# Performance work log

Hardware: AMD Instinct MI355X
Metric: run time of the kernel (lower is better)

## Reference

```python
import jax, jax.numpy as jnp
import numpy as np

ROPE_THETA = 500000.0


def apply_rope(x, position_ids):
    # x: (B, H, S, hd), position_ids: (B, S)
    hd = x.shape[-1]
    inv_freq = 1.0 / (ROPE_THETA ** (jnp.arange(0, hd, 2, dtype=x.dtype) / hd))  # (hd/2,)
    freqs = position_ids.astype(x.dtype)[:, :, None] * inv_freq  # (B, S, hd/2)
    sin = jnp.sin(freqs)[:, None, :, :]  # (B, 1, S, hd/2)
    cos = jnp.cos(freqs)[:, None, :, :]
    x1 = x[..., ::2]
    x2 = x[..., 1::2]
    even = x1 * cos - x2 * sin
    odd = x2 * cos + x1 * sin
    # interleave even/odd back: stack on a new trailing axis then flatten
    return jnp.stack([even, odd], axis=-1).reshape(x.shape)


def setup_inputs() -> dict:
    key = jax.random.key(0)
    k_x, k_q, k_k, k_v, k_o = jax.random.split(key, 5)
    B, S, D = 2, 2048, 2048
    H, H_kv = 32, 8
    hd = D // H
    x = jax.random.normal(k_x, (B, S, D), dtype=jnp.float32)
    position_ids = jnp.broadcast_to(jnp.arange(S, dtype=jnp.int64)[None, :], (B, S))
    scale = 0.02
    Wq = jax.random.normal(k_q, (D, H * hd), dtype=jnp.float32) * scale
    Wk = jax.random.normal(k_k, (D, H_kv * hd), dtype=jnp.float32) * scale
    Wv = jax.random.normal(k_v, (D, H_kv * hd), dtype=jnp.float32) * scale
    Wo = jax.random.normal(k_o, (D, D), dtype=jnp.float32) * scale
    return {"x": x, "position_ids": position_ids, "Wq": Wq, "Wk": Wk, "Wv": Wv, "Wo": Wo}


def reference(x, position_ids, Wq, Wk, Wv, Wo):
    B, S, D = x.shape
    H, H_kv = 32, 8
    hd = D // H
    G = H // H_kv  # query heads per kv head

    q = (x @ Wq).reshape(B, S, H, hd).transpose(0, 2, 1, 3)        # (B, H, S, hd)
    k = (x @ Wk).reshape(B, S, H_kv, hd).transpose(0, 2, 1, 3)     # (B, H_kv, S, hd)
    v = (x @ Wv).reshape(B, S, H_kv, hd).transpose(0, 2, 1, 3)

    q = apply_rope(q, position_ids)
    k = apply_rope(k, position_ids)

    # GQA: group query heads (B, H_kv, G, S, hd); repeat_interleave maps head h -> kv head h // G
    qg = q.reshape(B, H_kv, G, S, hd)
    scores = jnp.einsum("bkgsh,bkth->bkgst", qg, k) / jnp.sqrt(jnp.asarray(hd, x.dtype))

    causal = jnp.triu(jnp.ones((S, S), dtype=bool), 1)  # True = masked
    scores = jnp.where(causal, jnp.asarray(-jnp.inf, scores.dtype), scores)

    attn = jax.nn.softmax(scores, axis=-1)  # (B, H_kv, G, S, S)
    z = jnp.einsum("bkgst,bkth->bkgsh", attn, v)  # (B, H_kv, G, S, hd)
    z = z.reshape(B, H, S, hd).transpose(0, 2, 1, 3).reshape(B, S, D)
    return z @ Wo
```

## Files before the change

### kernel.cpp

```cpp
#include <hip/hip_runtime.h>
#include <hip/hip_bf16.h>


#define S_LEN 2048
#define DIM   2048
#define NH    32
#define NKV   8
#define HD    64
#define BS    4096
#define NQKV  3072
#define LL(x) ((long long)(x))

typedef __bf16 bf16x8 __attribute__((ext_vector_type(8)));
typedef float  f32x4  __attribute__((ext_vector_type(4)));
typedef float  f32x16 __attribute__((ext_vector_type(16)));
typedef unsigned u32x4 __attribute__((ext_vector_type(4)));

__device__ __forceinline__ unsigned short bfb(float f) {
  __hip_bfloat16 h = __float2bfloat16(f);
  return *reinterpret_cast<unsigned short*>(&h);
}

__device__ __forceinline__ unsigned cvtpk(float lo, float hi) {
  unsigned u;
  asm("v_cvt_pk_bf16_f32 %0, %1, %2" : "=v"(u) : "v"(lo), "v"(hi));
  return u;
}

__device__ __forceinline__ float fmax3(float a, float b, float c) {
  float d;
  asm("v_max3_f32 %0, %1, %2, %3" : "=v"(d) : "v"(a), "v"(b), "v"(c));
  return d;
}

__device__ __forceinline__ void gload16(const void* g, void* l) {
  __builtin_amdgcn_global_load_lds(
      (const __attribute__((address_space(1))) void*)g,
      (__attribute__((address_space(3))) void*)l, 16, 0, 0);
}

__device__ __forceinline__ void tcast_body(
    const float* __restrict__ in, unsigned short* __restrict__ out,
    int K, int N, int bx, int by, int tid, float* tile ) {
  int n0 = bx * 32, k0 = by * 32;
  int tx = tid & 31, ty = tid >> 5;
#pragma unroll
  for (int r = 0; r < 32; r += 8)
    tile[(ty + r) * 33 + tx] = in[LL(k0 + ty + r) * N + n0 + tx];
  __syncthreads();
#pragma unroll
  for (int r = 0; r < 32; r += 8)
    out[LL(n0 + ty + r) * K + k0 + tx] = bfb(tile[tx * 33 + ty + r]);
}

__global__ __launch_bounds__(256) void k_prep(
    const float* __restrict__ x,  const float* __restrict__ Wq,
    const float* __restrict__ Wk, const float* __restrict__ Wv,
    const float* __restrict__ Wo, float* __restrict__ tab,
    unsigned short* __restrict__ xb, unsigned short* __restrict__ wqkvt,
    unsigned short* __restrict__ wot) {
  __shared__ float tile[32 * 33];
  int blk = blockIdx.x, tid = threadIdx.x;
  if (blk < 256) {
    int i = blk * 256 + tid;
    int s = i >> 5, f = i & 31;
    double inv = pow(500000.0, -2.0 * (double)f / 64.0);
    double fr = (double)s * inv;
    tab[2 * i]     = (float)cos(fr);
    tab[2 * i + 1] = (float)sin(fr);
  } else if (blk < 8448) {
    int i = (blk - 256) * 256 + tid;
    float4 v = ((const float4*)x)[i];
    ushort4 o;
    o.x = bfb(v.x); o.y = bfb(v.y); o.z = bfb(v.z); o.w = bfb(v.w);
    ((ushort4*)xb)[i] = o;
  } else if (blk < 12544) {
    int t2 = blk - 8448;
    tcast_body(Wq, wqkvt, DIM, DIM, t2 & 63, t2 >> 6, tid, tile);
  } else if (blk < 13568) {
    int t3 = blk - 12544;
    tcast_body(Wk, wqkvt + LL(2048) * DIM, DIM, 512, t3 & 15, t3 >> 4, tid, tile);
  } else if (blk < 14592) {
    int t4 = blk - 13568;
    tcast_body(Wv, wqkvt + LL(2560) * DIM, DIM, 512, t4 & 15, t4 >> 4, tid, tile);
  } else {
    int t5 = blk - 14592;
    tcast_body(Wo, wot, DIM, DIM, t5 & 63, t5 >> 6, tid, tile);
  }
}

__global__ void k_vtrans(const unsigned short* __restrict__ vbuf, unsigned short* __restrict__ vt) {
  __shared__ __align__(16) unsigned short tile[64][72];
  int s0 = blockIdx.x * 64;
  int bh = blockIdx.y;
  int b = bh >> 3, kvh = bh & 7;
  int t = threadIdx.x;
#pragma unroll
  for (int c = t; c < 512; c += 256) {
    int s = c >> 3, seg = c & 7;
    *(uint4*)&tile[s][seg * 8] =
        *(const uint4*)(vbuf + LL(b * S_LEN + s0 + s) * (NKV * HD) + kvh * HD + seg * 8);
  }
  __syncthreads();
#pragma unroll
  for (int c = t; c < 512; c += 256) {
    int d = c >> 3, sseg = c & 7;
    ushort4 x0, x1;
    unsigned short* xp = (unsigned short*)&x0;
#pragma unroll
    for (int j = 0; j < 4; j++) xp[j] = tile[sseg * 8 + j][d];
    unsigned short* yp = (unsigned short*)&x1;
#pragma unroll
    for (int j = 0; j < 4; j++) yp[j] = tile[sseg * 8 + 4 + j][d];
    uint4 o;
    o.x = ((unsigned*)&x0)[0]; o.y = ((unsigned*)&x0)[1];
    o.z = ((unsigned*)&x1)[0]; o.w = ((unsigned*)&x1)[1];
    *(uint4*)(vt + (LL(bh) * HD + d) * S_LEN + s0 + sseg * 8) = o;
  }
}

template <int MODE>
__global__ __launch_bounds__(256, 2) void k_gemm(
    const unsigned short* __restrict__ A, const unsigned short* __restrict__ Bt,
    void* __restrict__ Cout, int M, int N, int K,
    const float* __restrict__ tab, unsigned short* __restrict__ qbuf,
    unsigned short* __restrict__ kbuf, unsigned short* __restrict__ vbuf) {
  __shared__ __align__(16) unsigned short As[128 * 32];
  __shared__ __align__(16) unsigned short Bs[128 * 32];
  int t = threadIdx.x;
  int lane = t & 63, w = t >> 6;
  int wr = w >> 1, wc = w & 1;
  int g = lane >> 4, r = lane & 15;
  int gx = gridDim.x;
  int nwg = gx * gridDim.y;
  int lin = blockIdx.y * gx + blockIdx.x;
  int cpx = nwg >> 3;
  int swz = (lin & 7) * cpx + (lin >> 3);
  int bx = swz % gx, by = swz / gx;
  long long rowBase = LL(by) * 128;
  long long colBase = LL(bx) * 128;

  f32x4 acc[4][4] = {};

  int c0 = t, c1 = t + 256;
  const unsigned short* ag0 = A + (rowBase + (c0 >> 2)) * K + (c0 & 3) * 8;
  const unsigned short* ag1 = A + (rowBase + (c1 >> 2)) * K + (c1 & 3) * 8;
  const unsigned short* bg0 = Bt + (colBase + (c0 >> 2)) * K + (c0 & 3) * 8;
  const unsigned short* bg1 = Bt + (colBase + (c1 >> 2)) * K + (c1 & 3) * 8;
  char* lA0 = (char*)As + c0 * 16; char* lA1 = (char*)As + c1 * 16;
  char* lB0 = (char*)Bs + c0 * 16; char* lB1 = (char*)Bs + c1 * 16;

  for (int kt = 0; kt < K; kt += 32) {
    __syncthreads();
    gload16(ag0 + kt, lA0);
    gload16(ag1 + kt, lA1);
    gload16(bg0 + kt, lB0);
    gload16(bg1 + kt, lB1);
    __syncthreads();

    bf16x8 af[4], bfr[4];
#pragma unroll
    for (int m = 0; m < 4; m++)
      af[m] = *(const bf16x8*)(const void*)(As + (wr * 64 + m * 16 + r) * 32 + g * 8);
#pragma unroll
    for (int n = 0; n < 4; n++)
      bfr[n] = *(const bf16x8*)(const void*)(Bs + (wc * 64 + n * 16 + r) * 32 + g * 8);
#pragma unroll
    for (int m = 0; m < 4; m++)
#pragma unroll
      for (int n = 0; n < 4; n++)
        acc[m][n] = __builtin_amdgcn_mfma_f32_16x16x32_bf16(af[m], bfr[n], acc[m][n], 0, 0, 0);
  }

  if (MODE == 0) {
#pragma unroll
    for (int m = 0; m < 4; m++)
#pragma unroll
      for (int n = 0; n < 4; n++) {
        long long row0 = rowBase + wr * 64 + m * 16 + g * 4;
        long long col = colBase + wc * 64 + n * 16 + r;
#pragma unroll
        for (int j = 0; j < 4; j++)
          ((float*)Cout)[(row0 + j) * N + col] = acc[m][n][j];
      }
  } else {
#pragma unroll
    for (int n = 0; n < 4; n++) {
      int gc0 = (int)colBase + wc * 64 + n * 16;
      int gc = gc0 + r;
      unsigned short* dst; int dcol, dstride; float scale; bool rope;
      if (gc0 < 2048)      { dst = qbuf; dcol = gc;        dstride = DIM; scale = 0.18033688f; rope = true; }
      else if (gc0 < 2560) { dst = kbuf; dcol = gc - 2048; dstride = 512; scale = 1.0f;        rope = true; }
      else                 { dst = vbuf; dcol = gc - 2560; dstride = 512; scale = 1.0f;        rope = false; }
      int f = (gc & 63) >> 1;
      float sgn = (gc & 1) ? 1.f : -1.f;
#pragma unroll
      for (int m = 0; m < 4; m++) {
        long long row0 = rowBase + wr * 64 + m * 16 + g * 4;
#pragma unroll
        for (int j = 0; j < 4; j++) {
          float v = acc[m][n][j];
          float o;
          if (rope) {
            float part = __shfl_xor(v, 1);
            int s = (int)((row0 + j) & (S_LEN - 1));
            float cc = tab[(s * 32 + f) * 2], ss = tab[(s * 32 + f) * 2 + 1];
            o = (v * cc + sgn * part * ss) * scale;
          } else o = v;
          dst[(row0 + j) * dstride + dcol] = bfb(o);
        }
      }
    }
  }
}

__global__ __launch_bounds__(256, 2) void k_attn(
    const unsigned short* __restrict__ qb, const unsigned short* __restrict__ kb,
    const unsigned short* __restrict__ vt, unsigned short* __restrict__ zb) {
  int lin = blockIdx.x + 8 * (blockIdx.y + 32 * blockIdx.z);
  int kvh = lin & 7;
  int idx = lin >> 3;
  int b = idx >> 5;
  int j = idx & 31;
  int h = kvh * 4 + (j & 3);
  int pair = j >> 2;
  int bh = b * NKV + kvh;

  int t = threadIdx.x, lane = t & 63, w = t >> 6;
  int l31 = lane & 31, hi = lane >> 5;
  int sw = (l31 & 7) * 8;

  __shared__ __align__(16) unsigned short Ks[2][64 * 64];
  __shared__ __align__(16) unsigned short Vs[2][64 * 64];

  int c0 = t, c1 = t + 256;
  const unsigned short* kg0 = kb + LL(b) * S_LEN * 512 + (c0 >> 3) * 512 + kvh * HD
                                 + (((c0 & 7) ^ ((c0 >> 3) & 7)) * 8);
  const unsigned short* kg1 = kb + LL(b) * S_LEN * 512 + (c1 >> 3) * 512 + kvh * HD
                                 + (((c1 & 7) ^ ((c1 >> 3) & 7)) * 8);
  const unsigned short* vg0 = vt + (LL(bh) * HD + (c0 >> 3)) * S_LEN
                                 + (((c0 & 7) ^ ((c0 >> 3) & 7)) * 8);
  const unsigned short* vg1 = vt + (LL(bh) * HD + (c1 >> 3)) * S_LEN
                                 + (((c1 & 7) ^ ((c1 >> 3) & 7)) * 8);

#define STAGE(bufi, kst_)                                              \
  {                                                                    \
    gload16(kg0 + LL(kst_) * 512, (char*)Ks[bufi] + c0 * 16);          \
    gload16(kg1 + LL(kst_) * 512, (char*)Ks[bufi] + c1 * 16);          \
    gload16(vg0 + (kst_), (char*)Vs[bufi] + c0 * 16);                  \
    gload16(vg1 + (kst_), (char*)Vs[bufi] + c1 * 16);                  \
  }

#pragma unroll 1
  for (int pass = 0; pass < 2; pass++) {
    int st = pass ? (15 - pair) : pair;
    int rowb = st * 128 + w * 32;
    int qg = rowb + l31;
    long long qrow = LL(b) * S_LEN + qg;

    bf16x8 qf[4];
#pragma unroll
    for (int s = 0; s < 4; s++)
      qf[s] = *(const bf16x8*)(const void*)(qb + qrow * DIM + h * HD + s * 16 + hi * 8);

    f32x16 acc0 = {}, acc1 = {};
    float mrun = -1e30f, lrun = 0.f;

    int nt = 2 * st + 2;
    __syncthreads();
    STAGE(0, 0);
    for (int tt = 0; tt < nt; tt++) {
      int kst = tt * 64;
      int cur = tt & 1;
      if (tt + 1 < nt) {
        STAGE(cur ^ 1, kst + 64);
        asm volatile("s_waitcnt vmcnt(4)" ::: "memory");
      } else {
        asm volatile("s_waitcnt vmcnt(0)" ::: "memory");
      }
      __builtin_amdgcn_s_barrier();
      __builtin_amdgcn_sched_barrier(0);

      if (kst <= rowb + 31) {
        const unsigned short* Kc = Ks[cur];
        const unsigned short* Vc = Vs[cur];

        bf16x8 kf[2][4];
#pragma unroll
        for (int kbi = 0; kbi < 2; kbi++)
#pragma unroll
          for (int s = 0; s < 4; s++)
            kf[kbi][s] = *(const bf16x8*)(const void*)(
                Kc + (kbi * 32 + l31) * 64 + ((s * 16 + hi * 8) ^ sw));

        __builtin_amdgcn_s_setprio(1);
        f32x16 sc0 = {}, sc1 = {};
#pragma unroll
        for (int s = 0; s < 4; s++) {
          sc0 = __builtin_amdgcn_mfma_f32_32x32x16_bf16(kf[0][s], qf[s], sc0, 0, 0, 0);
          sc1 = __builtin_amdgcn_mfma_f32_32x32x16_bf16(kf[1][s], qf[s], sc1, 0, 0, 0);
        }
        __builtin_amdgcn_s_setprio(0);

        bf16x8 vf[8];
#pragma unroll
        for (int db = 0; db < 2; db++)
#pragma unroll
          for (int f = 0; f < 4; f++)
            vf[db * 4 + f] = *(const bf16x8*)(const void*)(
                Vc + (db * 32 + l31) * 64 + ((f * 16 + hi * 8) ^ sw));

        if (kst + 63 > rowb) {
#pragma unroll
          for (int q = 0; q < 16; q++) {
            int kl = (q & 3) + 8 * (q >> 2) + 4 * hi;
            if (kst + kl > qg) sc0[q] = -1e30f;
            if (kst + 32 + kl > qg) sc1[q] = -1e30f;
          }
        }

        float tq[16];
#pragma unroll
        for (int q = 0; q < 16; q++) tq[q] = fmaxf(sc0[q], sc1[q]);
        float u0 = fmax3(tq[0], tq[1], tq[2]);
        float u1 = fmax3(tq[3], tq[4], tq[5]);
        float u2 = fmax3(tq[6], tq[7], tq[8]);
        float u3 = fmax3(tq[9], tq[10], tq[11]);
        float u4 = fmax3(tq[12], tq[13], tq[14]);
        float lpm = fmaxf(fmax3(u0, u1, u2), fmax3(u3, u4, tq[15]));
        if (__any(lpm > mrun + 12.0f)) {
          float pmr = fmaxf(lpm, __shfl_xor(lpm, 32));
          float mnew = fmaxf(mrun, pmr);
          float al = exp2f(mrun - mnew);
          mrun = mnew;
          lrun *= al;
          acc0 *= al;
          acc1 *= al;
        }
        f32x16 pv0, pv1;
#pragma unroll
        for (int q = 0; q < 16; q++) {
          pv0[q] = exp2f(sc0[q] - mrun);
          pv1[q] = exp2f(sc1[q] - mrun);
        }
        {
          float la = 0.f, lb = 0.f, lc = 0.f, ld = 0.f;
#pragma unroll
          for (int q = 0; q < 16; q += 4) {
            la += pv0[q];     lb += pv0[q + 1];
            lc += pv0[q + 2]; ld += pv0[q + 3];
            la += pv1[q];     lb += pv1[q + 1];
            lc += pv1[q + 2]; ld += pv1[q + 3];
          }
          lrun += (la + lb) + (lc + ld);
        }

        bf16x8 pfr[4];
#pragma unroll
        for (int f = 0; f < 4; f++) {
          int qb_ = (f & 1) * 8;
          float e0, e1, e2, e3, e4, e5, e6, e7;
          if (f < 2) {
            e0 = pv0[qb_ + 0]; e1 = pv0[qb_ + 1]; e2 = pv0[qb_ + 2]; e3 = pv0[qb_ + 3];
            e4 = pv0[qb_ + 4]; e5 = pv0[qb_ + 5]; e6 = pv0[qb_ + 6]; e7 = pv0[qb_ + 7];
          } else {
            e0 = pv1[qb_ + 0]; e1 = pv1[qb_ + 1]; e2 = pv1[qb_ + 2]; e3 = pv1[qb_ + 3];
            e4 = pv1[qb_ + 4]; e5 = pv1[qb_ + 5]; e6 = pv1[qb_ + 6]; e7 = pv1[qb_ + 7];
          }
          unsigned a0 = cvtpk(e0, e1), a1 = cvtpk(e2, e3);
          unsigned b0 = cvtpk(e4, e5), b1 = cvtpk(e6, e7);
          unsigned y0 = __shfl_xor(hi ? a0 : b0, 32);
          unsigned y1 = __shfl_xor(hi ? a1 : b1, 32);
          u32x4 uu;
          uu[0] = hi ? y0 : a0;
          uu[1] = hi ? y1 : a1;
          uu[2] = hi ? b0 : y0;
          uu[3] = hi ? b1 : y1;
          pfr[f] = *(bf16x8*)&uu;
        }

        __builtin_amdgcn_s_setprio(1);
#pragma unroll
        for (int f = 0; f < 4; f++) {
          acc0 = __builtin_amdgcn_mfma_f32_32x32x16_bf16(vf[f],     pfr[f], acc0, 0, 0, 0);
          acc1 = __builtin_amdgcn_mfma_f32_32x32x16_bf16(vf[4 + f], pfr[f], acc1, 0, 0, 0);
        }
        __builtin_amdgcn_s_setprio(0);
      }

      __builtin_amdgcn_sched_barrier(0);
      __builtin_amdgcn_s_barrier();
    }

    float lfull = lrun + __shfl_xor(lrun, 32);
    float invl = 1.0f / lfull;
#pragma unroll
    for (int q4 = 0; q4 < 4; q4++) {
      uint2 u;
      u.x = cvtpk(acc0[q4 * 4 + 0] * invl, acc0[q4 * 4 + 1] * invl);
      u.y = cvtpk(acc0[q4 * 4 + 2] * invl, acc0[q4 * 4 + 3] * invl);
      *(uint2*)(void*)(zb + qrow * DIM + h * HD + 8 * q4 + 4 * hi) = u;
      uint2 v;
      v.x = cvtpk(acc1[q4 * 4 + 0] * invl, acc1[q4 * 4 + 1] * invl);
      v.y = cvtpk(acc1[q4 * 4 + 2] * invl, acc1[q4 * 4 + 3] * invl);
      *(uint2*)(void*)(zb + qrow * DIM + h * HD + 32 + 8 * q4 + 4 * hi) = v;
    }
  }
#undef STAGE
}

extern "C" void kernel_launch(void* const* d_in, const int* in_sizes, int n_in,
                              void* d_out, int out_size, void* d_ws, size_t ws_size,
                              hipStream_t stream) {
  const float* x  = (const float*)d_in[0];
  const float* Wq = (const float*)d_in[2];
  const float* Wk = (const float*)d_in[3];
  const float* Wv = (const float*)d_in[4];
  const float* Wo = (const float*)d_in[5];
  float* out = (float*)d_out;

  char* wsb = (char*)d_ws;
  size_t off = 0;
  auto alloc = [&](size_t bytes) {
    void* p = wsb + off;
    off += (bytes + 255) & ~(size_t)255;
    return p;
  };
  float* tab            = (float*)alloc(LL(S_LEN) * 32 * 2 * 4);
  unsigned short* xb    = (unsigned short*)alloc(LL(BS) * DIM * 2);
  unsigned short* wqkvt = (unsigned short*)alloc(LL(NQKV) * DIM * 2);
  unsigned short* wot   = (unsigned short*)alloc(LL(DIM) * DIM * 2);
  unsigned short* qbuf  = (unsigned short*)alloc(LL(BS) * DIM * 2);
  unsigned short* kbuf  = (unsigned short*)alloc(LL(BS) * (NKV * HD) * 2);
  unsigned short* vbuf  = (unsigned short*)alloc(LL(BS) * (NKV * HD) * 2);
  unsigned short* vtb   = (unsigned short*)alloc(LL(2 * NKV) * HD * S_LEN * 2);
  unsigned short* zb    = (unsigned short*)alloc(LL(BS) * DIM * 2);

  k_prep<<<18688, 256, 0, stream>>>(x, Wq, Wk, Wv, Wo, tab, xb, wqkvt, wot);

  k_gemm<2><<<dim3(NQKV / 128, BS / 128), 256, 0, stream>>>(
      xb, wqkvt, nullptr, BS, NQKV, DIM, tab, qbuf, kbuf, vbuf);

  k_vtrans<<<dim3(S_LEN / 64, 2 * NKV), 256, 0, stream>>>(vbuf, vtb);

  k_attn<<<dim3(8, NH, 2), 256, 0, stream>>>(qbuf, kbuf, vtb, zb);

  k_gemm<0><<<dim3(DIM / 128, BS / 128), 256, 0, stream>>>(
      zb, wot, out, BS, DIM, DIM, nullptr, nullptr, nullptr, nullptr);
}
```

Baseline: 221.8 us.

## Fuse V transpose into QKV GEMM epilogue and simplify softmax max/sum reduction

The QKV projection epilogue now writes V directly in transposed (head, dim, seq) layout, which removes the separate k_vtrans kernel launch and the intermediate vbuf round trip. The transposed stores are strided by S_LEN per element, so the GEMM epilogue gets scattered 2-byte writes in place of row-contiguous ones. The attention softmax also replaces the max3 tree with a linear fmax chain, shuffles the row max before the rescale check, and reduces the row sum across half-waves on every tile instead of once at the end. That moves one shuffle per tile into the inner loop and lengthens the dependency chains.

```diff
diff --git a/kernel.cpp b/kernel.cpp
--- a/kernel.cpp
+++ b/kernel.cpp
@@ -25,12 +25,6 @@
   unsigned u;
   asm("v_cvt_pk_bf16_f32 %0, %1, %2" : "=v"(u) : "v"(lo), "v"(hi));
   return u;
-}
-
-__device__ __forceinline__ float fmax3(float a, float b, float c) {
-  float d;
-  asm("v_max3_f32 %0, %1, %2, %3" : "=v"(d) : "v"(a), "v"(b), "v"(c));
-  return d;
 }
 
 __device__ __forceinline__ void gload16(const void* g, void* l) {
@@ -89,42 +83,12 @@
   }
 }
 
-__global__ void k_vtrans(const unsigned short* __restrict__ vbuf, unsigned short* __restrict__ vt) {
-  __shared__ __align__(16) unsigned short tile[64][72];
-  int s0 = blockIdx.x * 64;
-  int bh = blockIdx.y;
-  int b = bh >> 3, kvh = bh & 7;
-  int t = threadIdx.x;
-#pragma unroll
-  for (int c = t; c < 512; c += 256) {
-    int s = c >> 3, seg = c & 7;
-    *(uint4*)&tile[s][seg * 8] =
-        *(const uint4*)(vbuf + LL(b * S_LEN + s0 + s) * (NKV * HD) + kvh * HD + seg * 8);
-  }
-  __syncthreads();
-#pragma unroll
-  for (int c = t; c < 512; c += 256) {
-    int d = c >> 3, sseg = c & 7;
-    ushort4 x0, x1;
-    unsigned short* xp = (unsigned short*)&x0;
-#pragma unroll
-    for (int j = 0; j < 4; j++) xp[j] = tile[sseg * 8 + j][d];
-    unsigned short* yp = (unsigned short*)&x1;
-#pragma unroll
-    for (int j = 0; j < 4; j++) yp[j] = tile[sseg * 8 + 4 + j][d];
-    uint4 o;
-    o.x = ((unsigned*)&x0)[0]; o.y = ((unsigned*)&x0)[1];
-    o.z = ((unsigned*)&x1)[0]; o.w = ((unsigned*)&x1)[1];
-    *(uint4*)(vt + (LL(bh) * HD + d) * S_LEN + s0 + sseg * 8) = o;
-  }
-}
-
 template <int MODE>
 __global__ __launch_bounds__(256, 2) void k_gemm(
     const unsigned short* __restrict__ A, const unsigned short* __restrict__ Bt,
     void* __restrict__ Cout, int M, int N, int K,
     const float* __restrict__ tab, unsigned short* __restrict__ qbuf,
-    unsigned short* __restrict__ kbuf, unsigned short* __restrict__ vbuf) {
+    unsigned short* __restrict__ kbuf, unsigned short* __restrict__ vtb) {
   __shared__ __align__(16) unsigned short As[128 * 32];
   __shared__ __align__(16) unsigned short Bs[128 * 32];
   int t = threadIdx.x;
@@ -188,26 +152,37 @@
     for (int n = 0; n < 4; n++) {
       int gc0 = (int)colBase + wc * 64 + n * 16;
       int gc = gc0 + r;
-      unsigned short* dst; int dcol, dstride; float scale; bool rope;
-      if (gc0 < 2048)      { dst = qbuf; dcol = gc;        dstride = DIM; scale = 0.18033688f; rope = true; }
-      else if (gc0 < 2560) { dst = kbuf; dcol = gc - 2048; dstride = 512; scale = 1.0f;        rope = true; }
-      else                 { dst = vbuf; dcol = gc - 2560; dstride = 512; scale = 1.0f;        rope = false; }
-      int f = (gc & 63) >> 1;
-      float sgn = (gc & 1) ? 1.f : -1.f;
-#pragma unroll
-      for (int m = 0; m < 4; m++) {
-        long long row0 = rowBase + wr * 64 + m * 16 + g * 4;
-#pragma unroll
-        for (int j = 0; j < 4; j++) {
-          float v = acc[m][n][j];
-          float o;
-          if (rope) {
+      if (gc0 < 2560) {
+        unsigned short* dst; int dcol, dstride; float scale;
+        if (gc0 < 2048) { dst = qbuf; dcol = gc;        dstride = DIM; scale = 0.18033688f; }
+        else            { dst = kbuf; dcol = gc - 2048; dstride = 512; scale = 1.0f; }
+        int f = (gc & 63) >> 1;
+        float sgn = (gc & 1) ? 1.f : -1.f;
+#pragma unroll
+        for (int m = 0; m < 4; m++) {
+          long long row0 = rowBase + wr * 64 + m * 16 + g * 4;
+#pragma unroll
+          for (int j = 0; j < 4; j++) {
+            float v = acc[m][n][j];
             float part = __shfl_xor(v, 1);
             int s = (int)((row0 + j) & (S_LEN - 1));
             float cc = tab[(s * 32 + f) * 2], ss = tab[(s * 32 + f) * 2 + 1];
-            o = (v * cc + sgn * part * ss) * scale;
-          } else o = v;
-          dst[(row0 + j) * dstride + dcol] = bfb(o);
+            float o = (v * cc + sgn * part * ss) * scale;
+            dst[(row0 + j) * dstride + dcol] = bfb(o);
+          }
+        }
+      } else {
+        int dcol = gc - 2560;
+#pragma unroll
+        for (int m = 0; m < 4; m++) {
+          long long row0 = rowBase + wr * 64 + m * 16 + g * 4;
+#pragma unroll
+          for (int j = 0; j < 4; j++) {
+            long long row = row0 + j;
+            long long bq = row >> 11;
+            int s = (int)(row & (S_LEN - 1));
+            vtb[(bq * 512 + dcol) * S_LEN + s] = bfb(acc[m][n][j]);
+          }
         }
       }
     }
@@ -319,18 +294,15 @@
           }
         }
 
-        float tq[16];
-#pragma unroll
-        for (int q = 0; q < 16; q++) tq[q] = fmaxf(sc0[q], sc1[q]);
-        float u0 = fmax3(tq[0], tq[1], tq[2]);
-        float u1 = fmax3(tq[3], tq[4], tq[5]);
-        float u2 = fmax3(tq[6], tq[7], tq[8]);
-        float u3 = fmax3(tq[9], tq[10], tq[11]);
-        float u4 = fmax3(tq[12], tq[13], tq[14]);
-        float lpm = fmaxf(fmax3(u0, u1, u2), fmax3(u3, u4, tq[15]));
-        if (__any(lpm > mrun + 12.0f)) {
-          float pmr = fmaxf(lpm, __shfl_xor(lpm, 32));
-          float mnew = fmaxf(mrun, pmr);
+        float pm = -1e30f;
+#pragma unroll
+        for (int q = 0; q < 16; q++) {
+          pm = fmaxf(pm, sc0[q]);
+          pm = fmaxf(pm, sc1[q]);
+        }
+        pm = fmaxf(pm, __shfl_xor(pm, 32));
+        if (__any(pm > mrun + 12.0f)) {
+          float mnew = fmaxf(mrun, pm);
           float al = exp2f(mrun - mnew);
           mrun = mnew;
           lrun *= al;
@@ -338,22 +310,14 @@
           acc1 *= al;
         }
         f32x16 pv0, pv1;
+        float ls = 0.f;
 #pragma unroll
         for (int q = 0; q < 16; q++) {
           pv0[q] = exp2f(sc0[q] - mrun);
           pv1[q] = exp2f(sc1[q] - mrun);
-        }
-        {
-          float la = 0.f, lb = 0.f, lc = 0.f, ld = 0.f;
-#pragma unroll
-          for (int q = 0; q < 16; q += 4) {
-            la += pv0[q];     lb += pv0[q + 1];
-            lc += pv0[q + 2]; ld += pv0[q + 3];
-            la += pv1[q];     lb += pv1[q + 1];
-            lc += pv1[q + 2]; ld += pv1[q + 3];
-          }
-          lrun += (la + lb) + (lc + ld);
-        }
+          ls += pv0[q] + pv1[q];
+        }
+        lrun += ls + __shfl_xor(ls, 32);
 
         bf16x8 pfr[4];
 #pragma unroll
@@ -392,8 +356,7 @@
       __builtin_amdgcn_s_barrier();
     }
 
-    float lfull = lrun + __shfl_xor(lrun, 32);
-    float invl = 1.0f / lfull;
+    float invl = 1.0f / lrun;
 #pragma unroll
     for (int q4 = 0; q4 < 4; q4++) {
       uint2 u;
@@ -432,16 +395,13 @@
   unsigned short* wot   = (unsigned short*)alloc(LL(DIM) * DIM * 2);
   unsigned short* qbuf  = (unsigned short*)alloc(LL(BS) * DIM * 2);
   unsigned short* kbuf  = (unsigned short*)alloc(LL(BS) * (NKV * HD) * 2);
-  unsigned short* vbuf  = (unsigned short*)alloc(LL(BS) * (NKV * HD) * 2);
   unsigned short* vtb   = (unsigned short*)alloc(LL(2 * NKV) * HD * S_LEN * 2);
   unsigned short* zb    = (unsigned short*)alloc(LL(BS) * DIM * 2);
 
   k_prep<<<18688, 256, 0, stream>>>(x, Wq, Wk, Wv, Wo, tab, xb, wqkvt, wot);
 
   k_gemm<2><<<dim3(NQKV / 128, BS / 128), 256, 0, stream>>>(
-      xb, wqkvt, nullptr, BS, NQKV, DIM, tab, qbuf, kbuf, vbuf);
-
-  k_vtrans<<<dim3(S_LEN / 64, 2 * NKV), 256, 0, stream>>>(vbuf, vtb);
+      xb, wqkvt, nullptr, BS, NQKV, DIM, tab, qbuf, kbuf, vtb);
 
   k_attn<<<dim3(8, NH, 2), 256, 0, stream>>>(qbuf, kbuf, vtb, zb);
 
```

Result: faster. 208.8 us (-5.9%).
